# Optimization experiments

Hardware: AMD Instinct MI355X
Metric: run time of the kernel (lower is better)

The kernel has to match this reference:

```python
import jax, jax.numpy as jnp
import numpy as np

EMBED_DIM = 2048
N_HEADS = 16
D_HEAD = EMBED_DIM // N_HEADS


def setup_inputs() -> dict:
    key = jax.random.key(0)
    kx, kq, kk, kv = jax.random.split(key, 4)
    B, N, D = 4, 2048, EMBED_DIM
    x = jax.random.normal(kx, (B, N, D), dtype=jnp.float32)
    Wq = jax.random.normal(kq, (D, D), dtype=jnp.float32) * 0.02
    Wk = jax.random.normal(kk, (D, D), dtype=jnp.float32) * 0.02
    Wv = jax.random.normal(kv, (D, D), dtype=jnp.float32) * 0.02
    return {"x": x, "Wq": Wq, "Wk": Wk, "Wv": Wv}


def reference(x, Wq, Wk, Wv):
    # x: [B, N, D]; weights applied as x @ W (matching torch.matmul in source)
    B, N, D = x.shape
    H, d = N_HEADS, D_HEAD
    # [B, N, D] -> [B, H, N, d]
    Q = (x @ Wq).reshape(B, N, H, d).transpose(0, 2, 1, 3)
    K = (x @ Wk).reshape(B, N, H, d).transpose(0, 2, 1, 3)
    V = (x @ Wv).reshape(B, N, H, d).transpose(0, 2, 1, 3)
    scale = 1.0 / jnp.sqrt(jnp.asarray(d, dtype=x.dtype))
    # non-causal SDPA (torch default: no mask, scale = 1/sqrt(d_head))
    scores = jnp.einsum('bhqd,bhkd->bhqk', Q, K) * scale  # [B,H,N,N]
    attn = jax.nn.softmax(scores, axis=-1)
    out = jnp.einsum('bhqk,bhkd->bhqd', attn, V)  # [B,H,N,d]
    return out
```

## Files before the change

### kernel.cpp

```cpp
#include <hip/hip_runtime.h>
#include <hip/hip_bf16.h>

#define B 4
#define N 2048
#define D 2048
#define H 16
#define DH 128
#define NT 32

typedef unsigned short u16;
typedef __attribute__((ext_vector_type(8))) short short8;
typedef __attribute__((ext_vector_type(4))) float floatx4;

__device__ __forceinline__ u16 f2b(float f) {
    union { __hip_bfloat16 h; u16 u; } cv;
    cv.h = __float2bfloat16(f);
    return cv.u;
}

__device__ __forceinline__ floatx4 mfma16(short8 a, short8 b, floatx4 c) {
    return __builtin_amdgcn_mfma_f32_16x16x32_bf16(a, b, c, 0, 0, 0);
}

#if __has_builtin(__builtin_amdgcn_exp2f)
#define EXP2(x) __builtin_amdgcn_exp2f(x)
#else
#define EXP2(x) exp2f(x)
#endif

__device__ __forceinline__ void async16(const void* g, void* l) {
    __builtin_amdgcn_global_load_lds(
        (const __attribute__((address_space(1))) unsigned int*)g,
        (__attribute__((address_space(3))) unsigned int*)l, 16, 0, 0);
}

__global__ __launch_bounds__(256) void cvt_fused(const float* __restrict__ x,
                                                 const float* __restrict__ Wq,
                                                 const float* __restrict__ Wk,
                                                 const float* __restrict__ Wv,
                                                 u16* __restrict__ xb,
                                                 u16* __restrict__ wt) {
    __shared__ float tile[64][65];
    const int bx = blockIdx.x;
    if (bx < 8192) {
        size_t i = ((size_t)bx * 256 + threadIdx.x) * 8;
        float4 v0 = *(const float4*)&x[i];
        float4 v1 = *(const float4*)&x[i + 4];
        union { u16 u[8]; uint4 s; } pk;
        pk.u[0] = f2b(v0.x); pk.u[1] = f2b(v0.y); pk.u[2] = f2b(v0.z); pk.u[3] = f2b(v0.w);
        pk.u[4] = f2b(v1.x); pk.u[5] = f2b(v1.y); pk.u[6] = f2b(v1.z); pk.u[7] = f2b(v1.w);
        *(uint4*)&xb[i] = pk.s;
        return;
    }
    const int wi = bx - 8192;
    const int z = wi >> 10;
    const int rem = wi & 1023;
    const float* W = (z == 0) ? Wq : (z == 1) ? Wk : Wv;
    const float scl = (z == 0) ? 0.12751743342f : 1.0f;
    const int k0 = (rem & 31) * 64, n0 = (rem >> 5) * 64;
    const int tr = threadIdx.x >> 4, tc = threadIdx.x & 15;
#pragma unroll
    for (int i = 0; i < 4; i++) {
        int kk = tr + 16 * i;
        float4 vv = *(const float4*)&W[(size_t)(k0 + kk) * D + n0 + tc * 4];
        tile[kk][tc * 4 + 0] = vv.x; tile[kk][tc * 4 + 1] = vv.y;
        tile[kk][tc * 4 + 2] = vv.z; tile[kk][tc * 4 + 3] = vv.w;
    }
    __syncthreads();
#pragma unroll
    for (int i = 0; i < 4; i++) {
        int nn = tr + 16 * i;
        union { u16 u[4]; ushort4 s; } pk;
#pragma unroll
        for (int j = 0; j < 4; j++) pk.u[j] = f2b(tile[tc * 4 + j][nn] * scl);
        *(ushort4*)&wt[(size_t)z * D * D + (size_t)(n0 + nn) * D + k0 + tc * 4] = pk.s;
    }
}

#define KT 32
#define SGB __builtin_amdgcn_sched_group_barrier
__global__ __launch_bounds__(512, 2) void qkv_gemm(const u16* __restrict__ xb,
                                                   const u16* __restrict__ wt,
                                                   u16* __restrict__ qo,
                                                   u16* __restrict__ ko,
                                                   u16* __restrict__ vo) {
    __shared__ u16 lds[81920];

    const int bid = blockIdx.x;
    const int c = bid & 7, i = bid >> 3;
    const int i6 = (i * 43) >> 8;
    const int tm = ((c >> 2) << 4) + i6;
    const int tn = (c & 3) * 6 + (i - 6 * i6);

    const int t = threadIdx.x, lane = t & 63, w = t >> 6;
    const int wr = w >> 2, wc = w & 3;
    const int q4 = lane >> 4, lr = lane & 15;

    const int m0 = tm * 256;
    const int n0 = tn * 256;

    unsigned aoff[2][2], boff[2][2];
#pragma unroll
    for (int ii = 0; ii < 2; ii++) {
        const int off = ii * 8192 + w * 1024 + lane * 16;
        const int row = off >> 7;
        const int s = (off >> 4) & 7;
        const int col = ((s ^ (row & 7))) * 8;
#pragma unroll
        for (int h = 0; h < 2; h++) {
            aoff[h][ii] = (unsigned)((m0 + h * 128 + row) * D + col);
            boff[h][ii] = (unsigned)((n0 + h * 128 + row) * D + col);
        }
    }

    const unsigned cb0 = (unsigned)(((0 * 4 + q4) ^ (lr & 7)) * 16);
    const unsigned cb1 = (unsigned)(((1 * 4 + q4) ^ (lr & 7)) * 16);
    const unsigned aC0 = (unsigned)(wr * 16384 + lr * 128) + cb0;
    const unsigned aC1 = (unsigned)(wr * 16384 + lr * 128) + cb1;
    const unsigned bC0 = (unsigned)((wc >> 1) * 16384 + (wc & 1) * 8192 + lr * 128) + cb0;
    const unsigned bC1 = (unsigned)((wc >> 1) * 16384 + (wc & 1) * 8192 + lr * 128) + cb1;

#define STAGE_A(bufoff, h, j) {                                                           \
    async16(xb + aoff[h][0] + (unsigned)(j) * 64,                                         \
            (char*)lds + (bufoff) + (h) * 16384 + w * 1024);                              \
    async16(xb + aoff[h][1] + (unsigned)(j) * 64,                                         \
            (char*)lds + (bufoff) + (h) * 16384 + 8192 + w * 1024); }
#define STAGE_B(bufoff, h, j) {                                                           \
    async16(wt + boff[h][0] + (unsigned)(j) * 64,                                         \
            (char*)lds + (bufoff) + (h) * 16384 + w * 1024);                              \
    async16(wt + boff[h][1] + (unsigned)(j) * 64,                                         \
            (char*)lds + (bufoff) + (h) * 16384 + 8192 + w * 1024); }
#define BAR() __builtin_amdgcn_s_barrier()
#define DSR(off) (*(const short8*)((const char*)lds + (off)))

    floatx4 acc[8][4];
#pragma unroll
    for (int x = 0; x < 8; x++)
#pragma unroll
        for (int j = 0; j < 4; j++) acc[x][j] = (floatx4){0.f, 0.f, 0.f, 0.f};

    STAGE_A(0u, 0, 0); STAGE_A(0u, 1, 0);
    STAGE_B(98304u, 0, 0); STAGE_B(98304u, 1, 0);
    STAGE_A(32768u, 0, 1); STAGE_A(32768u, 1, 1);
    asm volatile("s_waitcnt vmcnt(4)" ::: "memory");
    BAR();

    unsigned aOffR = 0u;
    unsigned aOffW = 65536u;

    for (int g = 0; g < KT; g++) {
        const unsigned bR = 98304u + (unsigned)((g & 1) << 15);
        const unsigned bW = 98304u + (unsigned)(((g + 1) & 1) << 15);

        if (g + 1 < KT) { STAGE_B(bW, 0, g + 1); STAGE_B(bW, 1, g + 1); }
        if (g + 2 < KT) { STAGE_A(aOffW, 0, g + 2); STAGE_A(aOffW, 1, g + 2); }
        __builtin_amdgcn_sched_barrier(0);

        const unsigned aB0 = aOffR + aC0, aB1 = aOffR + aC1;
        const unsigned bB0 = bR + bC0, bB1 = bR + bC1;

        short8 a0k0[4], a0k1[4], a1k0[4], a1k1[4];
        short8 b0k0[2], b0k1[2], b1k0[2], b1k1[2];

        b0k0[0] = DSR(bB0);        b0k0[1] = DSR(bB0 + 2048);
#pragma unroll
        for (int mf = 0; mf < 4; mf++) a0k0[mf] = DSR(aB0 + mf * 2048);
#pragma unroll
        for (int mf = 0; mf < 4; mf++) a1k0[mf] = DSR(aB0 + 8192 + mf * 2048);
#pragma unroll
        for (int nf = 0; nf < 2; nf++)
#pragma unroll
            for (int mf = 0; mf < 4; mf++)
                acc[mf][nf] = mfma16(a0k0[mf], b0k0[nf], acc[mf][nf]);
        b1k0[0] = DSR(bB0 + 4096); b1k0[1] = DSR(bB0 + 6144);
#pragma unroll
        for (int nf = 0; nf < 2; nf++)
#pragma unroll
            for (int mf = 0; mf < 4; mf++)
                acc[4 + mf][nf] = mfma16(a1k0[mf], b0k0[nf], acc[4 + mf][nf]);
        b0k1[0] = DSR(bB1);        b0k1[1] = DSR(bB1 + 2048);
#pragma unroll
        for (int mf = 0; mf < 4; mf++) a0k1[mf] = DSR(aB1 + mf * 2048);
#pragma unroll
        for (int nf = 0; nf < 2; nf++)
#pragma unroll
            for (int mf = 0; mf < 4; mf++)
                acc[4 + mf][2 + nf] = mfma16(a1k0[mf], b1k0[nf], acc[4 + mf][2 + nf]);
#pragma unroll
        for (int mf = 0; mf < 4; mf++) a1k1[mf] = DSR(aB1 + 8192 + mf * 2048);
#pragma unroll
        for (int nf = 0; nf < 2; nf++)
#pragma unroll
            for (int mf = 0; mf < 4; mf++)
                acc[mf][2 + nf] = mfma16(a0k0[mf], b1k0[nf], acc[mf][2 + nf]);
        b1k1[0] = DSR(bB1 + 4096); b1k1[1] = DSR(bB1 + 6144);
#pragma unroll
        for (int nf = 0; nf < 2; nf++)
#pragma unroll
            for (int mf = 0; mf < 4; mf++)
                acc[mf][nf] = mfma16(a0k1[mf], b0k1[nf], acc[mf][nf]);
#pragma unroll
        for (int nf = 0; nf < 2; nf++)
#pragma unroll
            for (int mf = 0; mf < 4; mf++)
                acc[4 + mf][nf] = mfma16(a1k1[mf], b0k1[nf], acc[4 + mf][nf]);
#pragma unroll
        for (int nf = 0; nf < 2; nf++)
#pragma unroll
            for (int mf = 0; mf < 4; mf++)
                acc[4 + mf][2 + nf] = mfma16(a1k1[mf], b1k1[nf], acc[4 + mf][2 + nf]);
#pragma unroll
        for (int nf = 0; nf < 2; nf++)
#pragma unroll
            for (int mf = 0; mf < 4; mf++)
                acc[mf][2 + nf] = mfma16(a0k1[mf], b1k1[nf], acc[mf][2 + nf]);

        SGB(0x100, 10, 0);
        SGB(0x008,  8, 0);
        SGB(0x100,  2, 0);
        SGB(0x008,  8, 0);
        SGB(0x100,  6, 0);
        SGB(0x008,  8, 0);
        SGB(0x100,  4, 0);
        SGB(0x008,  8, 0);
        SGB(0x100,  2, 0);
        SGB(0x008,  8, 0);
        SGB(0x008,  8, 0);
        SGB(0x008,  8, 0);
        SGB(0x008,  8, 0);

        if (g == KT - 2) { asm volatile("s_waitcnt vmcnt(0)" ::: "memory"); }
        else if (g < KT - 2) { asm volatile("s_waitcnt vmcnt(4)" ::: "memory"); }
        if (g + 1 < KT) BAR();

        aOffR = (aOffR == 65536u) ? 0u : aOffR + 32768u;
        aOffW = (aOffW == 65536u) ? 0u : aOffW + 32768u;
    }

    const int z = tn >> 3;
    if (z < 2) {
        u16* dst = (z == 0) ? qo : ko;
        const int c2b = (tn & 7) * 256 + wc * 64;
        const int grb = tm * 256 + wr * 128;
#pragma unroll
        for (int mf = 0; mf < 8; mf++)
#pragma unroll
            for (int nf = 0; nf < 4; nf++)
#pragma unroll
                for (int r = 0; r < 4; r++) {
                    int gr = grb + mf * 16 + q4 * 4 + r;
                    int c2 = c2b + nf * 16 + lr;
                    int b_ = gr >> 11, n_ = gr & (N - 1);
                    int head = c2 >> 7, dcol = c2 & 127;
                    dst[((size_t)(b_ * H + head) * N + n_) * DH + dcol] = f2b(acc[mf][nf][r]);
                }
    } else {
        __syncthreads();
        char* Vl = (char*)lds;
#pragma unroll
        for (int mf = 0; mf < 8; mf++) {
            const int granbase = wr * 32 + (mf >> 2) * 16 + ((mf & 3) >> 1) * 8
                               + ((mf & 3) & 1) + 2 * q4;
#pragma unroll
            for (int nf = 0; nf < 4; nf++) {
                int row = wc * 64 + nf * 16 + lr;
                union { u16 u[4]; unsigned long long qv; } pk;
#pragma unroll
                for (int r = 0; r < 4; r++) pk.u[r] = f2b(acc[mf][nf][r]);
                int gran = granbase ^ (row & 7);
                *(unsigned long long*)(Vl + row * 512 + gran * 8) = pk.qv;
            }
        }
        __syncthreads();
        const int bhb = (tm >> 3) * 16 + 2 * (tn & 7);
        const int nbase = (tm & 7) * 256;
#pragma unroll
        for (int pp = 0; pp < 32; pp++) {
            int idx = pp * 512 + t;
            int row = idx >> 6, g = idx & 63;
            unsigned long long v =
                *(const unsigned long long*)(Vl + row * 512 + ((g ^ (row & 7)) * 8));
            int bh = bhb + (row >> 7), dd = row & 127;
            *(unsigned long long*)&vo[((size_t)bh * DH + dd) * N + nbase + g * 4] = v;
        }
    }
#undef STAGE_A
#undef STAGE_B
#undef BAR
#undef DSR
}

#define FMAX2 17.312340491f
__global__ __launch_bounds__(256, 2) void attn_kernel(const u16* __restrict__ q,
                                                      const u16* __restrict__ k,
                                                      const u16* __restrict__ vt,
                                                      float* __restrict__ out) {
    __shared__ __align__(16) char smem[65536];

    const int beta = blockIdx.x;
    const int bh = (beta & 7) + 8 * (beta >> 7);
    const int qt = (beta >> 3) & 15;
    const int t = threadIdx.x;
    const int w = t >> 6, lane = t & 63;
    const int q4 = lane >> 4, lr = lane & 15;

    const size_t qbase = ((size_t)bh * N + (size_t)qt * 128) * DH;
    short8 af[2][4];
#pragma unroll
    for (int rt = 0; rt < 2; rt++)
#pragma unroll
        for (int ks = 0; ks < 4; ks++)
            af[rt][ks] = *(const short8*)&q[qbase + (size_t)(32 * w + 16 * rt + lr) * DH
                                            + ks * 32 + q4 * 8];

    float lrow[2] = {0.f, 0.f};
    floatx4 o[2][8];
#pragma unroll
    for (int rt = 0; rt < 2; rt++)
#pragma unroll
        for (int cv = 0; cv < 8; cv++) o[rt][cv] = (floatx4){0.f, 0.f, 0.f, 0.f};

    const u16* kpB = k + (size_t)bh * N * DH;
    const u16* vpB = vt + (size_t)bh * DH * N;
    unsigned koff[4], voff[4];
#pragma unroll
    for (int c = 0; c < 4; c++) {
        int grp = 4 * w + c;
        int krow = 4 * grp + (lane >> 4);
        int kg = (lane & 15) ^ (krow & 15);
        koff[c] = (unsigned)(krow * DH + kg * 8);
        int vrow = 8 * grp + (lane >> 3);
        int vg = (lane & 7) ^ (vrow & 7);
        voff[c] = (unsigned)(vrow * N + vg * 8);
    }

    unsigned kaddr[4];
#pragma unroll
    for (int ks = 0; ks < 4; ks++)
        kaddr[ks] = (unsigned)(lr * 256 + (((4 * ks + q4) ^ lr) * 16));
    unsigned vaddr[2];
#pragma unroll
    for (int a = 0; a < 2; a++)
        vaddr[a] = (unsigned)(32768 + lr * 128 + (((4 * a + q4) ^ (lr & 7)) * 16));

#pragma unroll
    for (int c = 0; c < 4; c++) {
        async16(kpB + koff[c], smem + (4 * w + c) * 1024);
        async16(vpB + voff[c], smem + 32768 + (4 * w + c) * 1024);
    }

    for (int kt = 0; kt < NT; kt++) {
        __syncthreads();

        if (kt + 1 < NT) {
            const int nb = (kt + 1) & 1;
#pragma unroll
            for (int c = 0; c < 4; c++) {
                async16(kpB + koff[c] + (unsigned)(kt + 1) * 64 * DH,
                        smem + nb * 16384 + (4 * w + c) * 1024);
                async16(vpB + voff[c] + (unsigned)(kt + 1) * 64,
                        smem + 32768 + nb * 16384 + (4 * w + c) * 1024);
            }
        }

        unsigned paw[2][4][2];
#pragma unroll
        for (int ct = 0; ct < 4; ct++) {
            short8 bf[4];
#pragma unroll
            for (int ks = 0; ks < 4; ks++)
                bf[ks] = *(const short8*)(smem + kaddr[ks] + ct * 4096);
#pragma unroll
            for (int rt = 0; rt < 2; rt++) {
                floatx4 s = (floatx4){0.f, 0.f, 0.f, 0.f};
#pragma unroll
                for (int ks = 0; ks < 4; ks++) s = mfma16(bf[ks], af[rt][ks], s);
                float p0 = EXP2(s[0] - FMAX2), p1 = EXP2(s[1] - FMAX2);
                float p2 = EXP2(s[2] - FMAX2), p3 = EXP2(s[3] - FMAX2);
                lrow[rt] += (p0 + p1) + (p2 + p3);
                paw[rt][ct][0] = (unsigned)f2b(p0) | ((unsigned)f2b(p1) << 16);
                paw[rt][ct][1] = (unsigned)f2b(p2) | ((unsigned)f2b(p3) << 16);
            }
        }
        short8 PA[2][2];
#pragma unroll
        for (int rt = 0; rt < 2; rt++)
#pragma unroll
            for (int a = 0; a < 2; a++) {
                union { unsigned uu[4]; short8 s8; } cv_;
                cv_.uu[0] = paw[rt][2 * a][0];     cv_.uu[1] = paw[rt][2 * a][1];
                cv_.uu[2] = paw[rt][2 * a + 1][0]; cv_.uu[3] = paw[rt][2 * a + 1][1];
                PA[rt][a] = cv_.s8;
            }

#pragma unroll
        for (int ctv = 0; ctv < 8; ctv++) {
#pragma unroll
            for (int a = 0; a < 2; a++) {
                short8 bv = *(const short8*)(smem + vaddr[a] + ctv * 2048);
#pragma unroll
                for (int rt = 0; rt < 2; rt++)
                    o[rt][ctv] = mfma16(PA[rt][a], bv, o[rt][ctv]);
            }
        }

#pragma unroll
        for (int ks = 0; ks < 4; ks++) kaddr[ks] ^= 16384u;
        vaddr[0] ^= 16384u; vaddr[1] ^= 16384u;
    }

    float* Ls = (float*)smem;
#pragma unroll
    for (int rt = 0; rt < 2; rt++) {
        float s = lrow[rt];
        s += __shfl_xor(s, 16);
        s += __shfl_xor(s, 32);
        if (q4 == 0) Ls[32 * w + 16 * rt + lr] = s;
    }
    __syncthreads();
    const size_t obase = ((size_t)bh * N + (size_t)qt * 128) * DH;
#pragma unroll
    for (int rt = 0; rt < 2; rt++) {
        floatx4 inv4;
#pragma unroll
        for (int r = 0; r < 4; r++)
            inv4[r] = 1.f / Ls[32 * w + 16 * rt + 4 * q4 + r];
#pragma unroll
        for (int ctv = 0; ctv < 8; ctv++) {
            int dd = 16 * ctv + lr;
#pragma unroll
            for (int r = 0; r < 4; r++) {
                int row = 32 * w + 16 * rt + 4 * q4 + r;
                out[obase + (size_t)row * DH + dd] = o[rt][ctv][r] * inv4[r];
            }
        }
    }
}

extern "C" void kernel_launch(void* const* d_in, const int* in_sizes, int n_in,
                              void* d_out, int out_size, void* d_ws, size_t ws_size,
                              hipStream_t stream) {
    const float* x  = (const float*)d_in[0];
    const float* Wq = (const float*)d_in[1];
    const float* Wk = (const float*)d_in[2];
    const float* Wv = (const float*)d_in[3];
    float* out = (float*)d_out;
    char* ws = (char*)d_ws;

    u16* xb = (u16*)(ws);
    u16* wt = (u16*)(ws + 33554432);
    u16* qb = (u16*)(ws + 58720256);
    u16* kb = (u16*)(ws + 92274688);
    u16* vtb = (u16*)(ws + 125829120);

    cvt_fused<<<dim3(11264), dim3(256), 0, stream>>>(x, Wq, Wk, Wv, xb, wt);
    qkv_gemm<<<dim3(768), dim3(512), 0, stream>>>(xb, wt, qb, kb, vtb);
    attn_kernel<<<dim3(1024), dim3(256), 0, stream>>>(qb, kb, vtb, out);
}
```

Before: 439.2 us.

## Software-pipeline QK^T of next tile with PV of previous tile using triple-buffered V

Restructures the attention main loop so the QK^T/exp for key tile i+1 is interleaved with the PV MFMAs for tile i, with a prologue and epilogue. V is now triple-buffered in shared memory (LDS grows from 64KB to 80KB) so the previous tile's V stays resident while the next ones load. The aim is to overlap the exp/convert latency with independent MFMA work. The larger LDS footprint may reduce the number of resident blocks per CU, and keeping P live across iterations adds register pressure.

```diff
diff --git a/kernel.cpp b/kernel.cpp
--- a/kernel.cpp
+++ b/kernel.cpp
@@ -295,7 +295,7 @@
                                                       const u16* __restrict__ k,
                                                       const u16* __restrict__ vt,
                                                       float* __restrict__ out) {
-    __shared__ __align__(16) char smem[65536];
+    __shared__ __align__(16) char smem[81920];
 
     const int beta = blockIdx.x;
     const int bh = (beta & 7) + 8 * (beta >> 7);
@@ -334,42 +334,36 @@
         voff[c] = (unsigned)(vrow * N + vg * 8);
     }
 
-    unsigned kaddr[4];
+    unsigned kaddrC[4];
 #pragma unroll
     for (int ks = 0; ks < 4; ks++)
-        kaddr[ks] = (unsigned)(lr * 256 + (((4 * ks + q4) ^ lr) * 16));
-    unsigned vaddr[2];
+        kaddrC[ks] = (unsigned)(lr * 256 + (((4 * ks + q4) ^ lr) * 16));
+    unsigned vaddrC[2];
 #pragma unroll
     for (int a = 0; a < 2; a++)
-        vaddr[a] = (unsigned)(32768 + lr * 128 + (((4 * a + q4) ^ (lr & 7)) * 16));
+        vaddrC[a] = (unsigned)(lr * 128 + (((4 * a + q4) ^ (lr & 7)) * 16));
 
 #pragma unroll
     for (int c = 0; c < 4; c++) {
         async16(kpB + koff[c], smem + (4 * w + c) * 1024);
         async16(vpB + voff[c], smem + 32768 + (4 * w + c) * 1024);
     }
-
-    for (int kt = 0; kt < NT; kt++) {
-        __syncthreads();
-
-        if (kt + 1 < NT) {
-            const int nb = (kt + 1) & 1;
-#pragma unroll
-            for (int c = 0; c < 4; c++) {
-                async16(kpB + koff[c] + (unsigned)(kt + 1) * 64 * DH,
-                        smem + nb * 16384 + (4 * w + c) * 1024);
-                async16(vpB + voff[c] + (unsigned)(kt + 1) * 64,
-                        smem + 32768 + nb * 16384 + (4 * w + c) * 1024);
-            }
-        }
-
+    __syncthreads();
+#pragma unroll
+    for (int c = 0; c < 4; c++) {
+        async16(kpB + koff[c] + 64 * DH, smem + 16384 + (4 * w + c) * 1024);
+        async16(vpB + voff[c] + 64, smem + 49152 + (4 * w + c) * 1024);
+    }
+
+    short8 PA[2][2];
+    {
         unsigned paw[2][4][2];
 #pragma unroll
         for (int ct = 0; ct < 4; ct++) {
             short8 bf[4];
 #pragma unroll
             for (int ks = 0; ks < 4; ks++)
-                bf[ks] = *(const short8*)(smem + kaddr[ks] + ct * 4096);
+                bf[ks] = *(const short8*)(smem + kaddrC[ks] + ct * 4096);
 #pragma unroll
             for (int rt = 0; rt < 2; rt++) {
                 floatx4 s = (floatx4){0.f, 0.f, 0.f, 0.f};
@@ -382,7 +376,6 @@
                 paw[rt][ct][1] = (unsigned)f2b(p2) | ((unsigned)f2b(p3) << 16);
             }
         }
-        short8 PA[2][2];
 #pragma unroll
         for (int rt = 0; rt < 2; rt++)
 #pragma unroll
@@ -392,21 +385,80 @@
                 cv_.uu[2] = paw[rt][2 * a + 1][0]; cv_.uu[3] = paw[rt][2 * a + 1][1];
                 PA[rt][a] = cv_.s8;
             }
-
-#pragma unroll
-        for (int ctv = 0; ctv < 8; ctv++) {
+    }
+
+    unsigned kRd = 16384u;
+    unsigned vRd = 32768u;
+    unsigned vWr = 65536u;
+
+    for (int i = 0; i < NT - 1; i++) {
+        __syncthreads();
+
+        if (i + 2 < NT) {
+#pragma unroll
+            for (int c = 0; c < 4; c++) {
+                async16(kpB + koff[c] + (unsigned)(i + 2) * 64 * DH,
+                        smem + (kRd ^ 16384u) + (4 * w + c) * 1024);
+                async16(vpB + voff[c] + (unsigned)(i + 2) * 64,
+                        smem + vWr + (4 * w + c) * 1024);
+            }
+        }
+
+        unsigned paw[2][4][2];
+#pragma unroll
+        for (int gq = 0; gq < 4; gq++) {
+            short8 bf[4];
+#pragma unroll
+            for (int ks = 0; ks < 4; ks++)
+                bf[ks] = *(const short8*)(smem + kRd + kaddrC[ks] + gq * 4096);
+#pragma unroll
+            for (int rt = 0; rt < 2; rt++) {
+                floatx4 s = (floatx4){0.f, 0.f, 0.f, 0.f};
+#pragma unroll
+                for (int ks = 0; ks < 4; ks++) s = mfma16(bf[ks], af[rt][ks], s);
+                float p0 = EXP2(s[0] - FMAX2), p1 = EXP2(s[1] - FMAX2);
+                float p2 = EXP2(s[2] - FMAX2), p3 = EXP2(s[3] - FMAX2);
+                lrow[rt] += (p0 + p1) + (p2 + p3);
+                paw[rt][gq][0] = (unsigned)f2b(p0) | ((unsigned)f2b(p1) << 16);
+                paw[rt][gq][1] = (unsigned)f2b(p2) | ((unsigned)f2b(p3) << 16);
+            }
+#pragma unroll
+            for (int cc = 0; cc < 2; cc++) {
+                const int ctv = 2 * gq + cc;
+#pragma unroll
+                for (int a = 0; a < 2; a++) {
+                    short8 bv = *(const short8*)(smem + vRd + vaddrC[a] + ctv * 2048);
+#pragma unroll
+                    for (int rt = 0; rt < 2; rt++)
+                        o[rt][ctv] = mfma16(PA[rt][a], bv, o[rt][ctv]);
+                }
+            }
+        }
+#pragma unroll
+        for (int rt = 0; rt < 2; rt++)
 #pragma unroll
             for (int a = 0; a < 2; a++) {
-                short8 bv = *(const short8*)(smem + vaddr[a] + ctv * 2048);
-#pragma unroll
-                for (int rt = 0; rt < 2; rt++)
-                    o[rt][ctv] = mfma16(PA[rt][a], bv, o[rt][ctv]);
-            }
-        }
-
-#pragma unroll
-        for (int ks = 0; ks < 4; ks++) kaddr[ks] ^= 16384u;
-        vaddr[0] ^= 16384u; vaddr[1] ^= 16384u;
+                union { unsigned uu[4]; short8 s8; } cv_;
+                cv_.uu[0] = paw[rt][2 * a][0];     cv_.uu[1] = paw[rt][2 * a][1];
+                cv_.uu[2] = paw[rt][2 * a + 1][0]; cv_.uu[3] = paw[rt][2 * a + 1][1];
+                PA[rt][a] = cv_.s8;
+            }
+
+        kRd ^= 16384u;
+        vRd = (vRd == 65536u) ? 32768u : vRd + 16384u;
+        vWr = (vWr == 65536u) ? 32768u : vWr + 16384u;
+    }
+
+    __syncthreads();
+#pragma unroll
+    for (int ctv = 0; ctv < 8; ctv++) {
+#pragma unroll
+        for (int a = 0; a < 2; a++) {
+            short8 bv = *(const short8*)(smem + vRd + vaddrC[a] + ctv * 2048);
+#pragma unroll
+            for (int rt = 0; rt < 2; rt++)
+                o[rt][ctv] = mfma16(PA[rt][a], bv, o[rt][ctv]);
+        }
     }
 
     float* Ls = (float*)smem;
```

Result: slower. 455.3 us (+3.7%).
